# Kernel optimization log

Measured on AMD Instinct MI355X. Metric: run time of the kernel, lower is better.

The kernel has to match this reference:

```python
import jax, jax.numpy as jnp
import numpy as np

N_EMBD = 126
N_HEADS = 6
HEAD_DIM = N_EMBD // N_HEADS  # 21


def setup_inputs() -> dict:
    key = jax.random.key(0)
    k1, k2, k3 = jax.random.split(key, 3)
    B, T = 8, 2048
    x = jax.random.normal(k1, (B, T, N_EMBD), dtype=jnp.float32)
    # torch Linear weights stored as (out, in); we store transposed (in, out) for x @ W
    w_attn = jax.random.normal(k2, (N_EMBD, 3 * N_EMBD), dtype=jnp.float32) * (1.0 / np.sqrt(N_EMBD))
    w_proj = jax.random.normal(k3, (N_EMBD, N_EMBD), dtype=jnp.float32) * (1.0 / np.sqrt(N_EMBD))
    return {"x": x, "w_attn": w_attn, "w_proj": w_proj}


def reference(x, w_attn, w_proj):
    B, T, C = x.shape
    qkv = x @ w_attn                      # [B, T, 3C]
    q, k, v = jnp.split(qkv, 3, axis=-1)  # each [B, T, C]

    def heads(t):  # [B,T,C] -> [B,H,T,hd]
        return t.reshape(B, T, N_HEADS, HEAD_DIM).transpose(0, 2, 1, 3)

    q, k, v = heads(q), heads(k), heads(v)
    scale = 1.0 / np.sqrt(HEAD_DIM).astype(np.float32)
    scores = jnp.einsum('bhqd,bhkd->bhqk', q, k) * scale  # [B,H,T,T]
    causal = jnp.tril(jnp.ones((T, T), dtype=bool))
    scores = jnp.where(causal, scores, jnp.finfo(scores.dtype).min)
    attn = jax.nn.softmax(scores, axis=-1)
    out = jnp.einsum('bhqk,bhkd->bhqd', attn, v)           # [B,H,T,hd]
    out = out.transpose(0, 2, 1, 3).reshape(B, T, C)
    return out @ w_proj
```

## Files before the change

kernel.cpp:

```cpp
#include <hip/hip_runtime.h>
#include <hip/hip_bf16.h>


#define B_ 8
#define T_ 2048
#define C_ 126
#define H_ 6
#define D_ 21
#define TC_ 378
#define KP_ 128
#define DP_ 32
#define M_ 16384
#define QSCALE 0.31481923469333463f

typedef __hip_bfloat16 bf16;
typedef __bf16 bf16_t;
typedef __bf16 bf16x8 __attribute__((ext_vector_type(8)));
typedef float f32x4 __attribute__((ext_vector_type(4)));

__device__ __forceinline__ float ldf(const bf16* p, long i) { return __bfloat162float(p[i]); }
__device__ __forceinline__ float ldf(const float* p, long i) { return p[i]; }
__device__ __forceinline__ void stf(bf16* p, long i, float v) { p[i] = __float2bfloat16(v); }
__device__ __forceinline__ void stf(float* p, long i, float v) { p[i] = v; }

__device__ __forceinline__ unsigned int ld2(const bf16* x, long i) {
  return *(const unsigned int*)((const unsigned short*)x + i);
}
__device__ __forceinline__ unsigned int ld2(const float* x, long i) {
  const float2 f = *(const float2*)(x + i);
  union { bf16_t b[2]; unsigned int u; } cv;
  cv.b[0] = (bf16_t)f.x; cv.b[1] = (bf16_t)f.y;
  return cv.u;
}

__device__ __forceinline__ void probe_dtype(const void* x, int tid, int* sflag) {
  if (tid < 64) {
    const unsigned int w = ((const unsigned int*)x)[tid * 97 + 13];
    const unsigned int e = (w >> 7) & 0xFF;
    const bool bflike = (e >= 115 && e <= 131) || ((w & 0x7FFFu) == 0);
    const unsigned long long mask = __ballot(bflike);
    if (tid == 0) *sflag = (__popcll(mask) >= 40) ? 1 : 0;
  }
  __syncthreads();
}

template <typename T>
__device__ __forceinline__ void prep_w_body(const T* __restrict__ wa,
                                            const T* __restrict__ wp,
                                            bf16_t* __restrict__ WTa,
                                            bf16_t* __restrict__ WTp) {
  const int stride = gridDim.x * blockDim.x;
  const int idx0 = blockIdx.x * blockDim.x + threadIdx.x;
  for (int i = idx0; i < 384 * KP_ + KP_ * KP_; i += stride) {
    if (i < 384 * KP_) {
      const int n = i >> 7, k = i & 127;
      WTa[i] = (k < C_ && n < TC_) ? (bf16_t)ldf(wa, (long)k * TC_ + n) : (bf16_t)0.f;
    } else {
      const int j = i - 384 * KP_;
      const int n = j >> 7, k = j & 127;
      WTp[j] = (k < C_ && n < C_) ? (bf16_t)ldf(wp, (long)k * C_ + n) : (bf16_t)0.f;
    }
  }
}

__global__ __launch_bounds__(256) void prep_w_kernel(
    const void* __restrict__ x, const void* __restrict__ wa,
    const void* __restrict__ wp, bf16_t* __restrict__ WTa,
    bf16_t* __restrict__ WTp) {
  __shared__ int sflag;
  probe_dtype(x, threadIdx.x, &sflag);
  if (sflag) prep_w_body<bf16>((const bf16*)wa, (const bf16*)wp, WTa, WTp);
  else       prep_w_body<float>((const float*)wa, (const float*)wp, WTa, WTp);
}

#define QS_ 40

template <typename T>
__device__ __forceinline__ void qkv_body(
    const T* __restrict__ x, const bf16_t* __restrict__ WT,
    bf16_t* __restrict__ Qb, bf16_t* __restrict__ Kb, bf16_t* __restrict__ VT,
    bf16_t* __restrict__ xs, bf16_t* __restrict__ qbuf,
    bf16_t* __restrict__ kbuf, bf16_t* __restrict__ vbuf) {
  const int m0 = blockIdx.x * 16;
  const int tid = threadIdx.x;
  for (int i = tid; i < 16 * 64; i += 256) {
    const int row = i >> 6, cp = i & 63;
    unsigned int v = 0;
    if (cp < 63) v = ld2(x, (long)(m0 + row) * C_ + 2 * cp);
    ((unsigned int*)xs)[i] = v;
  }
  for (int i = tid; i < 6 * 16 * 11; i += 256) {
    const int h = i / 176, rem = i - h * 176, t = rem / 11, d = 21 + rem % 11;
    qbuf[(h * 16 + t) * QS_ + d] = (bf16_t)0.f;
    kbuf[(h * 16 + t) * QS_ + d] = (bf16_t)0.f;
  }
  for (int i = tid; i < 6 * 11 * 16; i += 256) {
    const int h = i / 176, rem = i - h * 176, d = 21 + rem / 16, t = rem % 16;
    vbuf[(h * 32 + d) * 16 + t] = (d == 21) ? (bf16_t)1.f : (bf16_t)0.f;
  }
  __syncthreads();

  const int wv = tid >> 6, lane = tid & 63;
  const int lr = lane & 15, quad = lane >> 4;
  const bf16_t* ar = xs + lr * KP_ + quad * 8;
  const bf16x8 a0 = *(const bf16x8*)(ar);
  const bf16x8 a1 = *(const bf16x8*)(ar + 32);
  const bf16x8 a2 = *(const bf16x8*)(ar + 64);
  const bf16x8 a3 = *(const bf16x8*)(ar + 96);

  for (int nt = wv; nt < 24; nt += 4) {
    const int n0 = nt * 16;
    const bf16x8* bp = (const bf16x8*)(WT + (long)(n0 + lr) * KP_ + quad * 8);
    f32x4 acc = {0.f, 0.f, 0.f, 0.f};
    acc = __builtin_amdgcn_mfma_f32_16x16x32_bf16(a0, bp[0],  acc, 0, 0, 0);
    acc = __builtin_amdgcn_mfma_f32_16x16x32_bf16(a1, bp[4],  acc, 0, 0, 0);
    acc = __builtin_amdgcn_mfma_f32_16x16x32_bf16(a2, bp[8],  acc, 0, 0, 0);
    acc = __builtin_amdgcn_mfma_f32_16x16x32_bf16(a3, bp[12], acc, 0, 0, 0);

    const int c = n0 + lr;
    if (c < TC_) {
      const int which = c / C_;
      const int cc = c - which * C_;
      const int h = cc / D_, d = cc - h * D_;
#pragma unroll
      for (int r = 0; r < 4; ++r) {
        const int t = quad * 4 + r;
        if (which == 0)
          qbuf[(h * 16 + t) * QS_ + d] = (bf16_t)(acc[r] * QSCALE);
        else if (which == 1)
          kbuf[(h * 16 + t) * QS_ + d] = (bf16_t)acc[r];
        else
          vbuf[(h * 32 + d) * 16 + t] = (bf16_t)acc[r];
      }
    }
  }
  __syncthreads();

  const int b = m0 >> 11, t0 = m0 & 2047;
  for (int i = tid; i < 192; i += 256) {
    const int j = (i < 96) ? i : i - 96;
    const int h = j >> 4, t = j & 15;
    const int4* src = (const int4*)(((i < 96) ? qbuf : kbuf) + (h * 16 + t) * QS_);
    int4* dst = (int4*)((((i < 96) ? Qb : Kb)) + ((long)(b * H_ + h) * T_ + (t0 + t)) * DP_);
    dst[0] = src[0]; dst[1] = src[1]; dst[2] = src[2]; dst[3] = src[3];
  }
  for (int i = tid; i < 192; i += 256) {
    const int h = i >> 5, d = i & 31;
    const int4* src = (const int4*)(vbuf + (h * 32 + d) * 16);
    int4* dst = (int4*)(VT + ((long)(b * H_ + h) * DP_ + d) * T_ + t0);
    dst[0] = src[0]; dst[1] = src[1];
  }
}

__global__ __launch_bounds__(256) void qkv_mfma(
    const void* __restrict__ x, const bf16_t* __restrict__ WT,
    bf16_t* __restrict__ Qb, bf16_t* __restrict__ Kb, bf16_t* __restrict__ VT) {
  __shared__ __align__(16) bf16_t xs[16 * KP_];
  __shared__ __align__(16) bf16_t qbuf[6 * 16 * QS_];
  __shared__ __align__(16) bf16_t kbuf[6 * 16 * QS_];
  __shared__ __align__(16) bf16_t vbuf[6 * 32 * 16];
  __shared__ int sflag;
  probe_dtype(x, threadIdx.x, &sflag);
  if (sflag) qkv_body<bf16>((const bf16*)x, WT, Qb, Kb, VT, xs, qbuf, kbuf, vbuf);
  else       qkv_body<float>((const float*)x, WT, Qb, Kb, VT, xs, qbuf, kbuf, vbuf);
}

__global__ __launch_bounds__(256, 4) void attn_mfma(
    const bf16_t* __restrict__ Qb, const bf16_t* __restrict__ Kb,
    const bf16_t* __restrict__ VT, bf16_t* __restrict__ ATTp) {
  __shared__ __align__(16) float smem[4352];
  const int bh = blockIdx.x;
  const int pr = 63 - blockIdx.y;
  const int tid = threadIdx.x;
  const int wv = tid >> 6, lane = tid & 63;
  const int lr = lane & 15, quad = lane >> 4;
  const int q0 = pr * 32;
  const int mq = quad * 4;

  const bf16_t* Qbh = Qb + (long)bh * T_ * DP_;
  const bf16_t* Kbh = Kb + (long)bh * T_ * DP_;
  const bf16_t* VTbh = VT + (long)bh * DP_ * T_;

  const bf16x8 qf0 = *(const bf16x8*)(Qbh + (long)(q0 + lr) * DP_ + quad * 8);
  const bf16x8 qf1 = *(const bf16x8*)(Qbh + (long)(q0 + 16 + lr) * DP_ + quad * 8);

  f32x4 o00 = {0.f,0.f,0.f,0.f}, o01 = {0.f,0.f,0.f,0.f};
  f32x4 o10 = {0.f,0.f,0.f,0.f}, o11 = {0.f,0.f,0.f,0.f};
  bf16_t* plA0 = (bf16_t*)smem + wv * 2048;
  bf16_t* plA1 = plA0 + 512;
  bf16_t* plB0 = plA0 + 1024;
  bf16_t* plB1 = plA0 + 1536;
  const int rsw = ((lane ^ (lane >> 2)) << 3);
  const int wb0 = ((lr >> 3) << 4) + mq;

  int t = wv;
  for (; t + 4 <= pr; t += 8) {
    const int kbA = t * 32, kbB = (t + 4) * 32;
    const bf16x8 kA0 = *(const bf16x8*)(Kbh + (long)(kbA + lr) * DP_ + quad * 8);
    const bf16x8 kA1 = *(const bf16x8*)(Kbh + (long)(kbA + 16 + lr) * DP_ + quad * 8);
    const bf16x8 kB0 = *(const bf16x8*)(Kbh + (long)(kbB + lr) * DP_ + quad * 8);
    const bf16x8 kB1 = *(const bf16x8*)(Kbh + (long)(kbB + 16 + lr) * DP_ + quad * 8);
    const bf16x8 vA0 = *(const bf16x8*)(VTbh + (long)lr * T_ + kbA + quad * 8);
    const bf16x8 vA1 = *(const bf16x8*)(VTbh + (long)(16 + lr) * T_ + kbA + quad * 8);
    const bf16x8 vB0 = *(const bf16x8*)(VTbh + (long)lr * T_ + kbB + quad * 8);
    const bf16x8 vB1 = *(const bf16x8*)(VTbh + (long)(16 + lr) * T_ + kbB + quad * 8);

    f32x4 sA00 = {0.f,0.f,0.f,0.f}, sA01 = {0.f,0.f,0.f,0.f};
    f32x4 sA10 = {0.f,0.f,0.f,0.f}, sA11 = {0.f,0.f,0.f,0.f};
    f32x4 sB00 = {0.f,0.f,0.f,0.f}, sB01 = {0.f,0.f,0.f,0.f};
    f32x4 sB10 = {0.f,0.f,0.f,0.f}, sB11 = {0.f,0.f,0.f,0.f};
    sA00 = __builtin_amdgcn_mfma_f32_16x16x32_bf16(qf0, kA0, sA00, 0, 0, 0);
    sA01 = __builtin_amdgcn_mfma_f32_16x16x32_bf16(qf0, kA1, sA01, 0, 0, 0);
    sA10 = __builtin_amdgcn_mfma_f32_16x16x32_bf16(qf1, kA0, sA10, 0, 0, 0);
    sA11 = __builtin_amdgcn_mfma_f32_16x16x32_bf16(qf1, kA1, sA11, 0, 0, 0);
    sB00 = __builtin_amdgcn_mfma_f32_16x16x32_bf16(qf0, kB0, sB00, 0, 0, 0);
    sB01 = __builtin_amdgcn_mfma_f32_16x16x32_bf16(qf0, kB1, sB01, 0, 0, 0);
    sB10 = __builtin_amdgcn_mfma_f32_16x16x32_bf16(qf1, kB0, sB10, 0, 0, 0);
    sB11 = __builtin_amdgcn_mfma_f32_16x16x32_bf16(qf1, kB1, sB11, 0, 0, 0);

    if (t + 4 == pr) {
#pragma unroll
      for (int r = 0; r < 4; ++r) {
        if (lr > mq + r) { sB00[r] = -1e30f; sB11[r] = -1e30f; }
        sB01[r] = -1e30f;
      }
    }
#pragma unroll
    for (int r = 0; r < 4; ++r) {
      const int b0 = wb0 + r, b1 = b0 + 32;
      const int i0 = ((b0 ^ (b0 >> 2)) << 3) + (lr & 7);
      const int i1 = ((b1 ^ (b1 >> 2)) << 3) + (lr & 7);
      plA0[i0] = (bf16_t)exp2f(sA00[r]);
      plA0[i1] = (bf16_t)exp2f(sA01[r]);
      plA1[i0] = (bf16_t)exp2f(sA10[r]);
      plA1[i1] = (bf16_t)exp2f(sA11[r]);
      plB0[i0] = (bf16_t)exp2f(sB00[r]);
      plB0[i1] = (bf16_t)exp2f(sB01[r]);
      plB1[i0] = (bf16_t)exp2f(sB10[r]);
      plB1[i1] = (bf16_t)exp2f(sB11[r]);
    }
    __builtin_amdgcn_wave_barrier();
    const bf16x8 pfA0 = *(const bf16x8*)(plA0 + rsw);
    const bf16x8 pfA1 = *(const bf16x8*)(plA1 + rsw);
    const bf16x8 pfB0 = *(const bf16x8*)(plB0 + rsw);
    const bf16x8 pfB1 = *(const bf16x8*)(plB1 + rsw);
    __builtin_amdgcn_wave_barrier();

    o00 = __builtin_amdgcn_mfma_f32_16x16x32_bf16(pfA0, vA0, o00, 0, 0, 0);
    o01 = __builtin_amdgcn_mfma_f32_16x16x32_bf16(pfA0, vA1, o01, 0, 0, 0);
    o10 = __builtin_amdgcn_mfma_f32_16x16x32_bf16(pfA1, vA0, o10, 0, 0, 0);
    o11 = __builtin_amdgcn_mfma_f32_16x16x32_bf16(pfA1, vA1, o11, 0, 0, 0);
    o00 = __builtin_amdgcn_mfma_f32_16x16x32_bf16(pfB0, vB0, o00, 0, 0, 0);
    o01 = __builtin_amdgcn_mfma_f32_16x16x32_bf16(pfB0, vB1, o01, 0, 0, 0);
    o10 = __builtin_amdgcn_mfma_f32_16x16x32_bf16(pfB1, vB0, o10, 0, 0, 0);
    o11 = __builtin_amdgcn_mfma_f32_16x16x32_bf16(pfB1, vB1, o11, 0, 0, 0);
  }

  if (t <= pr) {
    const int kb = t * 32;
    const bf16x8 k0 = *(const bf16x8*)(Kbh + (long)(kb + lr) * DP_ + quad * 8);
    const bf16x8 k1 = *(const bf16x8*)(Kbh + (long)(kb + 16 + lr) * DP_ + quad * 8);
    const bf16x8 v0 = *(const bf16x8*)(VTbh + (long)lr * T_ + kb + quad * 8);
    const bf16x8 v1 = *(const bf16x8*)(VTbh + (long)(16 + lr) * T_ + kb + quad * 8);
    f32x4 s00 = {0.f,0.f,0.f,0.f}, s01 = {0.f,0.f,0.f,0.f};
    f32x4 s10 = {0.f,0.f,0.f,0.f}, s11 = {0.f,0.f,0.f,0.f};
    s00 = __builtin_amdgcn_mfma_f32_16x16x32_bf16(qf0, k0, s00, 0, 0, 0);
    s01 = __builtin_amdgcn_mfma_f32_16x16x32_bf16(qf0, k1, s01, 0, 0, 0);
    s10 = __builtin_amdgcn_mfma_f32_16x16x32_bf16(qf1, k0, s10, 0, 0, 0);
    s11 = __builtin_amdgcn_mfma_f32_16x16x32_bf16(qf1, k1, s11, 0, 0, 0);
    if (t == pr) {
#pragma unroll
      for (int r = 0; r < 4; ++r) {
        if (lr > mq + r) { s00[r] = -1e30f; s11[r] = -1e30f; }
        s01[r] = -1e30f;
      }
    }
#pragma unroll
    for (int r = 0; r < 4; ++r) {
      const int b0 = wb0 + r, b1 = b0 + 32;
      const int i0 = ((b0 ^ (b0 >> 2)) << 3) + (lr & 7);
      const int i1 = ((b1 ^ (b1 >> 2)) << 3) + (lr & 7);
      plA0[i0] = (bf16_t)exp2f(s00[r]);
      plA0[i1] = (bf16_t)exp2f(s01[r]);
      plA1[i0] = (bf16_t)exp2f(s10[r]);
      plA1[i1] = (bf16_t)exp2f(s11[r]);
    }
    __builtin_amdgcn_wave_barrier();
    const bf16x8 pf0 = *(const bf16x8*)(plA0 + rsw);
    const bf16x8 pf1 = *(const bf16x8*)(plA1 + rsw);
    __builtin_amdgcn_wave_barrier();
    o00 = __builtin_amdgcn_mfma_f32_16x16x32_bf16(pf0, v0, o00, 0, 0, 0);
    o01 = __builtin_amdgcn_mfma_f32_16x16x32_bf16(pf0, v1, o01, 0, 0, 0);
    o10 = __builtin_amdgcn_mfma_f32_16x16x32_bf16(pf1, v0, o10, 0, 0, 0);
    o11 = __builtin_amdgcn_mfma_f32_16x16x32_bf16(pf1, v1, o11, 0, 0, 0);
  }

  __syncthreads();
  {
    float* my = smem + (wv * 64 + lane) * 17;
#pragma unroll
    for (int j = 0; j < 4; ++j) {
      my[j]      = o00[j];
      my[4 + j]  = o01[j];
      my[8 + j]  = o10[j];
      my[12 + j] = o11[j];
    }
  }
  __syncthreads();

  if (wv == 0) {
    float tot[16];
#pragma unroll
    for (int j = 0; j < 16; ++j)
      tot[j] = smem[lane * 17 + j] + smem[(64 + lane) * 17 + j] +
               smem[(128 + lane) * 17 + j] + smem[(192 + lane) * 17 + j];
    const int b = bh / H_, h = bh - b * H_;
#pragma unroll
    for (int r = 0; r < 4; ++r) {
      const float rl0 = 1.f / __shfl(tot[4 + r],  (lane & 48) + 5, 64);
      const float rl1 = 1.f / __shfl(tot[12 + r], (lane & 48) + 5, 64);
      const int qA = q0 + mq + r, qB = qA + 16;
      bf16_t* opA = ATTp + (long)(b * T_ + qA) * KP_ + h * D_;
      bf16_t* opB = ATTp + (long)(b * T_ + qB) * KP_ + h * D_;
      opA[lr] = (bf16_t)(tot[r] * rl0);
      opB[lr] = (bf16_t)(tot[8 + r] * rl1);
      if (lr < 5) {
        opA[16 + lr] = (bf16_t)(tot[4 + r] * rl0);
        opB[16 + lr] = (bf16_t)(tot[12 + r] * rl1);
      }
    }
  }
}

__global__ __launch_bounds__(256) void proj_mfma(
    const void* __restrict__ x, const bf16_t* __restrict__ ATTp,
    const bf16_t* __restrict__ WT, void* __restrict__ out) {
  __shared__ int sflag;
  probe_dtype(x, threadIdx.x, &sflag);
  const int isbf = sflag;

  const int m0 = blockIdx.x * 16;
  const int tid = threadIdx.x;
  const int wv = tid >> 6, lane = tid & 63;
  const int lr = lane & 15, quad = lane >> 4;

  const bf16x8* ap = (const bf16x8*)(ATTp + (long)(m0 + lr) * KP_ + quad * 8);
  const bf16x8 a0 = ap[0], a1 = ap[4], a2 = ap[8], a3 = ap[12];

  for (int nt = wv; nt < 8; nt += 4) {
    const int n0 = nt * 16;
    const bf16x8* bp = (const bf16x8*)(WT + (long)(n0 + lr) * KP_ + quad * 8);
    f32x4 acc = {0.f, 0.f, 0.f, 0.f};
    acc = __builtin_amdgcn_mfma_f32_16x16x32_bf16(a0, bp[0],  acc, 0, 0, 0);
    acc = __builtin_amdgcn_mfma_f32_16x16x32_bf16(a1, bp[4],  acc, 0, 0, 0);
    acc = __builtin_amdgcn_mfma_f32_16x16x32_bf16(a2, bp[8],  acc, 0, 0, 0);
    acc = __builtin_amdgcn_mfma_f32_16x16x32_bf16(a3, bp[12], acc, 0, 0, 0);

    const int c = n0 + lr;
    if (c < C_) {
#pragma unroll
      for (int r = 0; r < 4; ++r) {
        const int m = m0 + quad * 4 + r;
        if (isbf) stf((bf16*)out,  (long)m * C_ + c, acc[r]);
        else      stf((float*)out, (long)m * C_ + c, acc[r]);
      }
    }
  }
}

extern "C" void kernel_launch(void* const* d_in, const int* in_sizes, int n_in,
                              void* d_out, int out_size, void* d_ws, size_t ws_size,
                              hipStream_t stream) {
  const void* x      = d_in[0];
  const void* w_attn = d_in[1];
  const void* w_proj = d_in[2];

  char* base = (char*)d_ws;
  const long QKV = (long)48 * T_ * DP_;
  bf16_t* Qb = (bf16_t*)(base + 256);
  bf16_t* Kb = Qb + QKV;
  bf16_t* VT = Kb + QKV;
  bf16_t* WTa  = VT + QKV;
  bf16_t* WTp  = WTa + 384 * KP_;
  bf16_t* ATTp = WTp + KP_ * KP_;

  prep_w_kernel<<<64, 256, 0, stream>>>(x, w_attn, w_proj, WTa, WTp);
  qkv_mfma<<<M_ / 16, 256, 0, stream>>>(x, WTa, Qb, Kb, VT);
  attn_mfma<<<dim3(48, 64), 256, 0, stream>>>(Qb, Kb, VT, ATTp);
  proj_mfma<<<M_ / 16, 256, 0, stream>>>(x, ATTp, WTp, d_out);
}
```

Measured before the change: 135.4 us.

## Enlarge qkv/proj row tiles, stage proj output in LDS, tile weight transpose

The weight-prep kernel now transposes via a padded shared-memory tile so global reads and writes are coalesced. The QKV kernel processes 32 rows per block instead of 16, halving the block count and reusing weight fetches across two M tiles. The projection kernel handles 64 rows per block, stages results in LDS and writes contiguous vectorized output. The staging rounds fp32 outputs to bf16, which loses precision for float outputs.

```diff
diff --git a/kernel.cpp b/kernel.cpp
--- a/kernel.cpp
+++ b/kernel.cpp
@@ -48,18 +48,31 @@
 __device__ __forceinline__ void prep_w_body(const T* __restrict__ wa,
                                             const T* __restrict__ wp,
                                             bf16_t* __restrict__ WTa,
-                                            bf16_t* __restrict__ WTp) {
-  const int stride = gridDim.x * blockDim.x;
-  const int idx0 = blockIdx.x * blockDim.x + threadIdx.x;
-  for (int i = idx0; i < 384 * KP_ + KP_ * KP_; i += stride) {
-    if (i < 384 * KP_) {
-      const int n = i >> 7, k = i & 127;
-      WTa[i] = (k < C_ && n < TC_) ? (bf16_t)ldf(wa, (long)k * TC_ + n) : (bf16_t)0.f;
-    } else {
-      const int j = i - 384 * KP_;
-      const int n = j >> 7, k = j & 127;
-      WTp[j] = (k < C_ && n < C_) ? (bf16_t)ldf(wp, (long)k * C_ + n) : (bf16_t)0.f;
-    }
+                                            bf16_t* __restrict__ WTp,
+                                            float (*tile)[65]) {
+  const int id = blockIdx.x;
+  const bool isA = id < 12;
+  const int nt = isA ? (id % 6) : ((id - 12) & 1);
+  const int kt = isA ? (id / 6) : ((id - 12) >> 1);
+  const T* src = isA ? wa : wp;
+  bf16_t* dst = isA ? WTa : WTp;
+  const int NN = isA ? TC_ : C_;
+  const int NR = isA ? 384 : KP_;
+  const int tid = threadIdx.x;
+  const int wv = tid >> 6, lane = tid & 63;
+
+#pragma unroll
+  for (int rr = 0; rr < 16; ++rr) {
+    const int kl = wv * 16 + rr;
+    const int k = kt * 64 + kl, n = nt * 64 + lane;
+    tile[kl][lane] = (k < C_ && n < NN) ? ldf(src, (long)k * NN + n) : 0.f;
+  }
+  __syncthreads();
+#pragma unroll
+  for (int rr = 0; rr < 16; ++rr) {
+    const int nl = wv * 16 + rr;
+    const int n = nt * 64 + nl;
+    if (n < NR) dst[(long)n * KP_ + kt * 64 + lane] = (bf16_t)tile[lane][nl];
   }
 }
 
@@ -67,10 +80,11 @@
     const void* __restrict__ x, const void* __restrict__ wa,
     const void* __restrict__ wp, bf16_t* __restrict__ WTa,
     bf16_t* __restrict__ WTp) {
+  __shared__ float tile[64][65];
   __shared__ int sflag;
   probe_dtype(x, threadIdx.x, &sflag);
-  if (sflag) prep_w_body<bf16>((const bf16*)wa, (const bf16*)wp, WTa, WTp);
-  else       prep_w_body<float>((const float*)wa, (const float*)wp, WTa, WTp);
+  if (sflag) prep_w_body<bf16>((const bf16*)wa, (const bf16*)wp, WTa, WTp, tile);
+  else       prep_w_body<float>((const float*)wa, (const float*)wp, WTa, WTp, tile);
 }
 
 #define QS_ 40
@@ -81,34 +95,35 @@
     bf16_t* __restrict__ Qb, bf16_t* __restrict__ Kb, bf16_t* __restrict__ VT,
     bf16_t* __restrict__ xs, bf16_t* __restrict__ qbuf,
     bf16_t* __restrict__ kbuf, bf16_t* __restrict__ vbuf) {
-  const int m0 = blockIdx.x * 16;
+  const int m0 = blockIdx.x * 32;
   const int tid = threadIdx.x;
-  for (int i = tid; i < 16 * 64; i += 256) {
+  for (int i = tid; i < 32 * 64; i += 256) {
     const int row = i >> 6, cp = i & 63;
     unsigned int v = 0;
     if (cp < 63) v = ld2(x, (long)(m0 + row) * C_ + 2 * cp);
     ((unsigned int*)xs)[i] = v;
   }
-  for (int i = tid; i < 6 * 16 * 11; i += 256) {
-    const int h = i / 176, rem = i - h * 176, t = rem / 11, d = 21 + rem % 11;
-    qbuf[(h * 16 + t) * QS_ + d] = (bf16_t)0.f;
-    kbuf[(h * 16 + t) * QS_ + d] = (bf16_t)0.f;
-  }
-  for (int i = tid; i < 6 * 11 * 16; i += 256) {
-    const int h = i / 176, rem = i - h * 176, d = 21 + rem / 16, t = rem % 16;
-    vbuf[(h * 32 + d) * 16 + t] = (d == 21) ? (bf16_t)1.f : (bf16_t)0.f;
+  for (int i = tid; i < 6 * 32 * 11; i += 256) {
+    const int h = i / 352, rem = i - h * 352, t = rem / 11, d = 21 + rem % 11;
+    qbuf[(h * 32 + t) * QS_ + d] = (bf16_t)0.f;
+    kbuf[(h * 32 + t) * QS_ + d] = (bf16_t)0.f;
+  }
+  for (int i = tid; i < 6 * 11 * 32; i += 256) {
+    const int h = i / 352, rem = i - h * 352, d = 21 + rem / 32, t = rem & 31;
+    vbuf[(h * 32 + d) * 32 + t] = (d == 21) ? (bf16_t)1.f : (bf16_t)0.f;
   }
   __syncthreads();
 
   const int wv = tid >> 6, lane = tid & 63;
   const int lr = lane & 15, quad = lane >> 4;
-  const bf16_t* ar = xs + lr * KP_ + quad * 8;
+  const int mt = wv >> 1;
+  const bf16_t* ar = xs + (mt * 16 + lr) * KP_ + quad * 8;
   const bf16x8 a0 = *(const bf16x8*)(ar);
   const bf16x8 a1 = *(const bf16x8*)(ar + 32);
   const bf16x8 a2 = *(const bf16x8*)(ar + 64);
   const bf16x8 a3 = *(const bf16x8*)(ar + 96);
 
-  for (int nt = wv; nt < 24; nt += 4) {
+  for (int nt = (wv & 1); nt < 24; nt += 2) {
     const int n0 = nt * 16;
     const bf16x8* bp = (const bf16x8*)(WT + (long)(n0 + lr) * KP_ + quad * 8);
     f32x4 acc = {0.f, 0.f, 0.f, 0.f};
@@ -124,41 +139,41 @@
       const int h = cc / D_, d = cc - h * D_;
 #pragma unroll
       for (int r = 0; r < 4; ++r) {
-        const int t = quad * 4 + r;
+        const int t = mt * 16 + quad * 4 + r;
         if (which == 0)
-          qbuf[(h * 16 + t) * QS_ + d] = (bf16_t)(acc[r] * QSCALE);
+          qbuf[(h * 32 + t) * QS_ + d] = (bf16_t)(acc[r] * QSCALE);
         else if (which == 1)
-          kbuf[(h * 16 + t) * QS_ + d] = (bf16_t)acc[r];
+          kbuf[(h * 32 + t) * QS_ + d] = (bf16_t)acc[r];
         else
-          vbuf[(h * 32 + d) * 16 + t] = (bf16_t)acc[r];
+          vbuf[(h * 32 + d) * 32 + t] = (bf16_t)acc[r];
       }
     }
   }
   __syncthreads();
 
   const int b = m0 >> 11, t0 = m0 & 2047;
-  for (int i = tid; i < 192; i += 256) {
-    const int j = (i < 96) ? i : i - 96;
-    const int h = j >> 4, t = j & 15;
-    const int4* src = (const int4*)(((i < 96) ? qbuf : kbuf) + (h * 16 + t) * QS_);
-    int4* dst = (int4*)((((i < 96) ? Qb : Kb)) + ((long)(b * H_ + h) * T_ + (t0 + t)) * DP_);
+  for (int i = tid; i < 384; i += 256) {
+    const int j = (i < 192) ? i : i - 192;
+    const int h = j >> 5, t = j & 31;
+    const int4* src = (const int4*)(((i < 192) ? qbuf : kbuf) + (h * 32 + t) * QS_);
+    int4* dst = (int4*)((((i < 192) ? Qb : Kb)) + ((long)(b * H_ + h) * T_ + (t0 + t)) * DP_);
     dst[0] = src[0]; dst[1] = src[1]; dst[2] = src[2]; dst[3] = src[3];
   }
   for (int i = tid; i < 192; i += 256) {
     const int h = i >> 5, d = i & 31;
-    const int4* src = (const int4*)(vbuf + (h * 32 + d) * 16);
+    const int4* src = (const int4*)(vbuf + (h * 32 + d) * 32);
     int4* dst = (int4*)(VT + ((long)(b * H_ + h) * DP_ + d) * T_ + t0);
-    dst[0] = src[0]; dst[1] = src[1];
+    dst[0] = src[0]; dst[1] = src[1]; dst[2] = src[2]; dst[3] = src[3];
   }
 }
 
 __global__ __launch_bounds__(256) void qkv_mfma(
     const void* __restrict__ x, const bf16_t* __restrict__ WT,
     bf16_t* __restrict__ Qb, bf16_t* __restrict__ Kb, bf16_t* __restrict__ VT) {
-  __shared__ __align__(16) bf16_t xs[16 * KP_];
-  __shared__ __align__(16) bf16_t qbuf[6 * 16 * QS_];
-  __shared__ __align__(16) bf16_t kbuf[6 * 16 * QS_];
-  __shared__ __align__(16) bf16_t vbuf[6 * 32 * 16];
+  __shared__ __align__(16) bf16_t xs[32 * KP_];
+  __shared__ __align__(16) bf16_t qbuf[6 * 32 * QS_];
+  __shared__ __align__(16) bf16_t kbuf[6 * 32 * QS_];
+  __shared__ __align__(16) bf16_t vbuf[6 * 32 * 32];
   __shared__ int sflag;
   probe_dtype(x, threadIdx.x, &sflag);
   if (sflag) qkv_body<bf16>((const bf16*)x, WT, Qb, Kb, VT, xs, qbuf, kbuf, vbuf);
@@ -332,22 +347,25 @@
   }
 }
 
+#define OS_ 136
 __global__ __launch_bounds__(256) void proj_mfma(
     const void* __restrict__ x, const bf16_t* __restrict__ ATTp,
     const bf16_t* __restrict__ WT, void* __restrict__ out) {
+  __shared__ __align__(16) bf16_t obuf[64 * OS_];
   __shared__ int sflag;
   probe_dtype(x, threadIdx.x, &sflag);
   const int isbf = sflag;
 
-  const int m0 = blockIdx.x * 16;
+  const int m0 = blockIdx.x * 64;
   const int tid = threadIdx.x;
   const int wv = tid >> 6, lane = tid & 63;
   const int lr = lane & 15, quad = lane >> 4;
 
-  const bf16x8* ap = (const bf16x8*)(ATTp + (long)(m0 + lr) * KP_ + quad * 8);
+  const bf16x8* ap = (const bf16x8*)(ATTp + (long)(m0 + wv * 16 + lr) * KP_ + quad * 8);
   const bf16x8 a0 = ap[0], a1 = ap[4], a2 = ap[8], a3 = ap[12];
 
-  for (int nt = wv; nt < 8; nt += 4) {
+#pragma unroll
+  for (int nt = 0; nt < 8; ++nt) {
     const int n0 = nt * 16;
     const bf16x8* bp = (const bf16x8*)(WT + (long)(n0 + lr) * KP_ + quad * 8);
     f32x4 acc = {0.f, 0.f, 0.f, 0.f};
@@ -355,15 +373,23 @@
     acc = __builtin_amdgcn_mfma_f32_16x16x32_bf16(a1, bp[4],  acc, 0, 0, 0);
     acc = __builtin_amdgcn_mfma_f32_16x16x32_bf16(a2, bp[8],  acc, 0, 0, 0);
     acc = __builtin_amdgcn_mfma_f32_16x16x32_bf16(a3, bp[12], acc, 0, 0, 0);
-
-    const int c = n0 + lr;
-    if (c < C_) {
-#pragma unroll
-      for (int r = 0; r < 4; ++r) {
-        const int m = m0 + quad * 4 + r;
-        if (isbf) stf((bf16*)out,  (long)m * C_ + c, acc[r]);
-        else      stf((float*)out, (long)m * C_ + c, acc[r]);
-      }
+#pragma unroll
+    for (int r = 0; r < 4; ++r)
+      obuf[(wv * 16 + quad * 4 + r) * OS_ + n0 + lr] = (bf16_t)acc[r];
+  }
+  __syncthreads();
+
+  for (int i = tid; i < 64 * 63; i += 256) {
+    const int row = i / 63, c2 = i - row * 63;
+    const bf16_t* s = obuf + row * OS_ + 2 * c2;
+    if (isbf) {
+      union { bf16_t b[2]; unsigned int u; } cv;
+      cv.b[0] = s[0]; cv.b[1] = s[1];
+      ((unsigned int*)out)[(long)(m0 + row) * 63 + c2] = cv.u;
+    } else {
+      float2 f;
+      f.x = (float)s[0]; f.y = (float)s[1];
+      ((float2*)out)[(long)(m0 + row) * 63 + c2] = f;
     }
   }
 }
@@ -384,8 +410,8 @@
   bf16_t* WTp  = WTa + 384 * KP_;
   bf16_t* ATTp = WTp + KP_ * KP_;
 
-  prep_w_kernel<<<64, 256, 0, stream>>>(x, w_attn, w_proj, WTa, WTp);
-  qkv_mfma<<<M_ / 16, 256, 0, stream>>>(x, WTa, Qb, Kb, VT);
+  prep_w_kernel<<<16, 256, 0, stream>>>(x, w_attn, w_proj, WTa, WTp);
+  qkv_mfma<<<M_ / 32, 256, 0, stream>>>(x, WTa, Qb, Kb, VT);
   attn_mfma<<<dim3(48, 64), 256, 0, stream>>>(Qb, Kb, VT, ATTp);
-  proj_mfma<<<M_ / 16, 256, 0, stream>>>(x, ATTp, WTp, d_out);
-}
+  proj_mfma<<<M_ / 64, 256, 0, stream>>>(x, ATTp, WTp, d_out);
+}
```

After: 141.8 us. 1.05x slower.

## Pair causal query tiles per block for balanced work and cheaper bf16 rounding

Applied to the files above, without the earlier changes.

Each attention block now handles two query tiles, pr = 63-y and pr = y, so every block does roughly the same amount of causal work, and the grid is halved to 48x32. This targets the load imbalance and tail effect that came from giving short and long causal rows to separate blocks. The P-matrix conversion also switches from the bf16 cast to a hand-written round-half-up bit trick (no NaN handling) written as ushort into shared memory. The cost is fewer blocks in flight, a serial pass over both tiles, and an extra barrier between the passes.

```diff
diff --git a/kernel.cpp b/kernel.cpp
--- a/kernel.cpp
+++ b/kernel.cpp
@@ -12,6 +12,7 @@
 #define DP_ 32
 #define M_ 16384
 #define QSCALE 0.31481923469333463f
+#define QS_ 40
 
 typedef __hip_bfloat16 bf16;
 typedef __bf16 bf16_t;
@@ -31,6 +32,11 @@
   union { bf16_t b[2]; unsigned int u; } cv;
   cv.b[0] = (bf16_t)f.x; cv.b[1] = (bf16_t)f.y;
   return cv.u;
+}
+
+__device__ __forceinline__ unsigned short f2b(float f) {
+  union { float f; unsigned int u; } v; v.f = f;
+  return (unsigned short)((v.u + 0x8000u) >> 16);
 }
 
 __device__ __forceinline__ void probe_dtype(const void* x, int tid, int* sflag) {
@@ -73,8 +79,6 @@
   else       prep_w_body<float>((const float*)wa, (const float*)wp, WTa, WTp);
 }
 
-#define QS_ 40
-
 template <typename T>
 __device__ __forceinline__ void qkv_body(
     const T* __restrict__ x, const bf16_t* __restrict__ WT,
@@ -170,165 +174,173 @@
     const bf16_t* __restrict__ VT, bf16_t* __restrict__ ATTp) {
   __shared__ __align__(16) float smem[4352];
   const int bh = blockIdx.x;
-  const int pr = 63 - blockIdx.y;
+  const int cc_ = blockIdx.y;
   const int tid = threadIdx.x;
   const int wv = tid >> 6, lane = tid & 63;
   const int lr = lane & 15, quad = lane >> 4;
-  const int q0 = pr * 32;
   const int mq = quad * 4;
 
   const bf16_t* Qbh = Qb + (long)bh * T_ * DP_;
   const bf16_t* Kbh = Kb + (long)bh * T_ * DP_;
   const bf16_t* VTbh = VT + (long)bh * DP_ * T_;
 
-  const bf16x8 qf0 = *(const bf16x8*)(Qbh + (long)(q0 + lr) * DP_ + quad * 8);
-  const bf16x8 qf1 = *(const bf16x8*)(Qbh + (long)(q0 + 16 + lr) * DP_ + quad * 8);
-
-  f32x4 o00 = {0.f,0.f,0.f,0.f}, o01 = {0.f,0.f,0.f,0.f};
-  f32x4 o10 = {0.f,0.f,0.f,0.f}, o11 = {0.f,0.f,0.f,0.f};
-  bf16_t* plA0 = (bf16_t*)smem + wv * 2048;
-  bf16_t* plA1 = plA0 + 512;
-  bf16_t* plB0 = plA0 + 1024;
-  bf16_t* plB1 = plA0 + 1536;
+  unsigned short* plA0 = (unsigned short*)smem + wv * 2048;
+  unsigned short* plA1 = plA0 + 512;
+  unsigned short* plB0 = plA0 + 1024;
+  unsigned short* plB1 = plA0 + 1536;
   const int rsw = ((lane ^ (lane >> 2)) << 3);
   const int wb0 = ((lr >> 3) << 4) + mq;
 
-  int t = wv;
-  for (; t + 4 <= pr; t += 8) {
-    const int kbA = t * 32, kbB = (t + 4) * 32;
-    const bf16x8 kA0 = *(const bf16x8*)(Kbh + (long)(kbA + lr) * DP_ + quad * 8);
-    const bf16x8 kA1 = *(const bf16x8*)(Kbh + (long)(kbA + 16 + lr) * DP_ + quad * 8);
-    const bf16x8 kB0 = *(const bf16x8*)(Kbh + (long)(kbB + lr) * DP_ + quad * 8);
-    const bf16x8 kB1 = *(const bf16x8*)(Kbh + (long)(kbB + 16 + lr) * DP_ + quad * 8);
-    const bf16x8 vA0 = *(const bf16x8*)(VTbh + (long)lr * T_ + kbA + quad * 8);
-    const bf16x8 vA1 = *(const bf16x8*)(VTbh + (long)(16 + lr) * T_ + kbA + quad * 8);
-    const bf16x8 vB0 = *(const bf16x8*)(VTbh + (long)lr * T_ + kbB + quad * 8);
-    const bf16x8 vB1 = *(const bf16x8*)(VTbh + (long)(16 + lr) * T_ + kbB + quad * 8);
-
-    f32x4 sA00 = {0.f,0.f,0.f,0.f}, sA01 = {0.f,0.f,0.f,0.f};
-    f32x4 sA10 = {0.f,0.f,0.f,0.f}, sA11 = {0.f,0.f,0.f,0.f};
-    f32x4 sB00 = {0.f,0.f,0.f,0.f}, sB01 = {0.f,0.f,0.f,0.f};
-    f32x4 sB10 = {0.f,0.f,0.f,0.f}, sB11 = {0.f,0.f,0.f,0.f};
-    sA00 = __builtin_amdgcn_mfma_f32_16x16x32_bf16(qf0, kA0, sA00, 0, 0, 0);
-    sA01 = __builtin_amdgcn_mfma_f32_16x16x32_bf16(qf0, kA1, sA01, 0, 0, 0);
-    sA10 = __builtin_amdgcn_mfma_f32_16x16x32_bf16(qf1, kA0, sA10, 0, 0, 0);
-    sA11 = __builtin_amdgcn_mfma_f32_16x16x32_bf16(qf1, kA1, sA11, 0, 0, 0);
-    sB00 = __builtin_amdgcn_mfma_f32_16x16x32_bf16(qf0, kB0, sB00, 0, 0, 0);
-    sB01 = __builtin_amdgcn_mfma_f32_16x16x32_bf16(qf0, kB1, sB01, 0, 0, 0);
-    sB10 = __builtin_amdgcn_mfma_f32_16x16x32_bf16(qf1, kB0, sB10, 0, 0, 0);
-    sB11 = __builtin_amdgcn_mfma_f32_16x16x32_bf16(qf1, kB1, sB11, 0, 0, 0);
-
-    if (t + 4 == pr) {
+  const int prs[2] = {63 - cc_, cc_};
+#pragma unroll
+  for (int uj = 0; uj < 2; ++uj) {
+    const int pr = prs[uj];
+    const int q0 = pr * 32;
+
+    const bf16x8 qf0 = *(const bf16x8*)(Qbh + (long)(q0 + lr) * DP_ + quad * 8);
+    const bf16x8 qf1 = *(const bf16x8*)(Qbh + (long)(q0 + 16 + lr) * DP_ + quad * 8);
+
+    f32x4 o00 = {0.f,0.f,0.f,0.f}, o01 = {0.f,0.f,0.f,0.f};
+    f32x4 o10 = {0.f,0.f,0.f,0.f}, o11 = {0.f,0.f,0.f,0.f};
+
+    int t = wv;
+    for (; t + 4 <= pr; t += 8) {
+      const int kbA = t * 32, kbB = (t + 4) * 32;
+      const bf16x8 kA0 = *(const bf16x8*)(Kbh + (long)(kbA + lr) * DP_ + quad * 8);
+      const bf16x8 kA1 = *(const bf16x8*)(Kbh + (long)(kbA + 16 + lr) * DP_ + quad * 8);
+      const bf16x8 kB0 = *(const bf16x8*)(Kbh + (long)(kbB + lr) * DP_ + quad * 8);
+      const bf16x8 kB1 = *(const bf16x8*)(Kbh + (long)(kbB + 16 + lr) * DP_ + quad * 8);
+      const bf16x8 vA0 = *(const bf16x8*)(VTbh + (long)lr * T_ + kbA + quad * 8);
+      const bf16x8 vA1 = *(const bf16x8*)(VTbh + (long)(16 + lr) * T_ + kbA + quad * 8);
+      const bf16x8 vB0 = *(const bf16x8*)(VTbh + (long)lr * T_ + kbB + quad * 8);
+      const bf16x8 vB1 = *(const bf16x8*)(VTbh + (long)(16 + lr) * T_ + kbB + quad * 8);
+
+      f32x4 sA00 = {0.f,0.f,0.f,0.f}, sA01 = {0.f,0.f,0.f,0.f};
+      f32x4 sA10 = {0.f,0.f,0.f,0.f}, sA11 = {0.f,0.f,0.f,0.f};
+      f32x4 sB00 = {0.f,0.f,0.f,0.f}, sB01 = {0.f,0.f,0.f,0.f};
+      f32x4 sB10 = {0.f,0.f,0.f,0.f}, sB11 = {0.f,0.f,0.f,0.f};
+      sA00 = __builtin_amdgcn_mfma_f32_16x16x32_bf16(qf0, kA0, sA00, 0, 0, 0);
+      sA01 = __builtin_amdgcn_mfma_f32_16x16x32_bf16(qf0, kA1, sA01, 0, 0, 0);
+      sA10 = __builtin_amdgcn_mfma_f32_16x16x32_bf16(qf1, kA0, sA10, 0, 0, 0);
+      sA11 = __builtin_amdgcn_mfma_f32_16x16x32_bf16(qf1, kA1, sA11, 0, 0, 0);
+      sB00 = __builtin_amdgcn_mfma_f32_16x16x32_bf16(qf0, kB0, sB00, 0, 0, 0);
+      sB01 = __builtin_amdgcn_mfma_f32_16x16x32_bf16(qf0, kB1, sB01, 0, 0, 0);
+      sB10 = __builtin_amdgcn_mfma_f32_16x16x32_bf16(qf1, kB0, sB10, 0, 0, 0);
+      sB11 = __builtin_amdgcn_mfma_f32_16x16x32_bf16(qf1, kB1, sB11, 0, 0, 0);
+
+      if (t + 4 == pr) {
+#pragma unroll
+        for (int r = 0; r < 4; ++r) {
+          if (lr > mq + r) { sB00[r] = -1e30f; sB11[r] = -1e30f; }
+          sB01[r] = -1e30f;
+        }
+      }
 #pragma unroll
       for (int r = 0; r < 4; ++r) {
-        if (lr > mq + r) { sB00[r] = -1e30f; sB11[r] = -1e30f; }
-        sB01[r] = -1e30f;
-      }
-    }
-#pragma unroll
-    for (int r = 0; r < 4; ++r) {
-      const int b0 = wb0 + r, b1 = b0 + 32;
-      const int i0 = ((b0 ^ (b0 >> 2)) << 3) + (lr & 7);
-      const int i1 = ((b1 ^ (b1 >> 2)) << 3) + (lr & 7);
-      plA0[i0] = (bf16_t)exp2f(sA00[r]);
-      plA0[i1] = (bf16_t)exp2f(sA01[r]);
-      plA1[i0] = (bf16_t)exp2f(sA10[r]);
-      plA1[i1] = (bf16_t)exp2f(sA11[r]);
-      plB0[i0] = (bf16_t)exp2f(sB00[r]);
-      plB0[i1] = (bf16_t)exp2f(sB01[r]);
-      plB1[i0] = (bf16_t)exp2f(sB10[r]);
-      plB1[i1] = (bf16_t)exp2f(sB11[r]);
-    }
-    __builtin_amdgcn_wave_barrier();
-    const bf16x8 pfA0 = *(const bf16x8*)(plA0 + rsw);
-    const bf16x8 pfA1 = *(const bf16x8*)(plA1 + rsw);
-    const bf16x8 pfB0 = *(const bf16x8*)(plB0 + rsw);
-    const bf16x8 pfB1 = *(const bf16x8*)(plB1 + rsw);
-    __builtin_amdgcn_wave_barrier();
-
-    o00 = __builtin_amdgcn_mfma_f32_16x16x32_bf16(pfA0, vA0, o00, 0, 0, 0);
-    o01 = __builtin_amdgcn_mfma_f32_16x16x32_bf16(pfA0, vA1, o01, 0, 0, 0);
-    o10 = __builtin_amdgcn_mfma_f32_16x16x32_bf16(pfA1, vA0, o10, 0, 0, 0);
-    o11 = __builtin_amdgcn_mfma_f32_16x16x32_bf16(pfA1, vA1, o11, 0, 0, 0);
-    o00 = __builtin_amdgcn_mfma_f32_16x16x32_bf16(pfB0, vB0, o00, 0, 0, 0);
-    o01 = __builtin_amdgcn_mfma_f32_16x16x32_bf16(pfB0, vB1, o01, 0, 0, 0);
-    o10 = __builtin_amdgcn_mfma_f32_16x16x32_bf16(pfB1, vB0, o10, 0, 0, 0);
-    o11 = __builtin_amdgcn_mfma_f32_16x16x32_bf16(pfB1, vB1, o11, 0, 0, 0);
-  }
-
-  if (t <= pr) {
-    const int kb = t * 32;
-    const bf16x8 k0 = *(const bf16x8*)(Kbh + (long)(kb + lr) * DP_ + quad * 8);
-    const bf16x8 k1 = *(const bf16x8*)(Kbh + (long)(kb + 16 + lr) * DP_ + quad * 8);
-    const bf16x8 v0 = *(const bf16x8*)(VTbh + (long)lr * T_ + kb + quad * 8);
-    const bf16x8 v1 = *(const bf16x8*)(VTbh + (long)(16 + lr) * T_ + kb + quad * 8);
-    f32x4 s00 = {0.f,0.f,0.f,0.f}, s01 = {0.f,0.f,0.f,0.f};
-    f32x4 s10 = {0.f,0.f,0.f,0.f}, s11 = {0.f,0.f,0.f,0.f};
-    s00 = __builtin_amdgcn_mfma_f32_16x16x32_bf16(qf0, k0, s00, 0, 0, 0);
-    s01 = __builtin_amdgcn_mfma_f32_16x16x32_bf16(qf0, k1, s01, 0, 0, 0);
-    s10 = __builtin_amdgcn_mfma_f32_16x16x32_bf16(qf1, k0, s10, 0, 0, 0);
-    s11 = __builtin_amdgcn_mfma_f32_16x16x32_bf16(qf1, k1, s11, 0, 0, 0);
-    if (t == pr) {
+        const int b0 = wb0 + r, b1 = b0 + 32;
+        const int i0 = ((b0 ^ (b0 >> 2)) << 3) + (lr & 7);
+        const int i1 = ((b1 ^ (b1 >> 2)) << 3) + (lr & 7);
+        plA0[i0] = f2b(exp2f(sA00[r]));
+        plA0[i1] = f2b(exp2f(sA01[r]));
+        plA1[i0] = f2b(exp2f(sA10[r]));
+        plA1[i1] = f2b(exp2f(sA11[r]));
+        plB0[i0] = f2b(exp2f(sB00[r]));
+        plB0[i1] = f2b(exp2f(sB01[r]));
+        plB1[i0] = f2b(exp2f(sB10[r]));
+        plB1[i1] = f2b(exp2f(sB11[r]));
+      }
+      __builtin_amdgcn_wave_barrier();
+      const bf16x8 pfA0 = *(const bf16x8*)(plA0 + rsw);
+      const bf16x8 pfA1 = *(const bf16x8*)(plA1 + rsw);
+      const bf16x8 pfB0 = *(const bf16x8*)(plB0 + rsw);
+      const bf16x8 pfB1 = *(const bf16x8*)(plB1 + rsw);
+      __builtin_amdgcn_wave_barrier();
+
+      o00 = __builtin_amdgcn_mfma_f32_16x16x32_bf16(pfA0, vA0, o00, 0, 0, 0);
+      o01 = __builtin_amdgcn_mfma_f32_16x16x32_bf16(pfA0, vA1, o01, 0, 0, 0);
+      o10 = __builtin_amdgcn_mfma_f32_16x16x32_bf16(pfA1, vA0, o10, 0, 0, 0);
+      o11 = __builtin_amdgcn_mfma_f32_16x16x32_bf16(pfA1, vA1, o11, 0, 0, 0);
+      o00 = __builtin_amdgcn_mfma_f32_16x16x32_bf16(pfB0, vB0, o00, 0, 0, 0);
+      o01 = __builtin_amdgcn_mfma_f32_16x16x32_bf16(pfB0, vB1, o01, 0, 0, 0);
+      o10 = __builtin_amdgcn_mfma_f32_16x16x32_bf16(pfB1, vB0, o10, 0, 0, 0);
+      o11 = __builtin_amdgcn_mfma_f32_16x16x32_bf16(pfB1, vB1, o11, 0, 0, 0);
+    }
+
+    if (t <= pr) {
+      const int kb = t * 32;
+      const bf16x8 k0 = *(const bf16x8*)(Kbh + (long)(kb + lr) * DP_ + quad * 8);
+      const bf16x8 k1 = *(const bf16x8*)(Kbh + (long)(kb + 16 + lr) * DP_ + quad * 8);
+      const bf16x8 v0 = *(const bf16x8*)(VTbh + (long)lr * T_ + kb + quad * 8);
+      const bf16x8 v1 = *(const bf16x8*)(VTbh + (long)(16 + lr) * T_ + kb + quad * 8);
+      f32x4 s00 = {0.f,0.f,0.f,0.f}, s01 = {0.f,0.f,0.f,0.f};
+      f32x4 s10 = {0.f,0.f,0.f,0.f}, s11 = {0.f,0.f,0.f,0.f};
+      s00 = __builtin_amdgcn_mfma_f32_16x16x32_bf16(qf0, k0, s00, 0, 0, 0);
+      s01 = __builtin_amdgcn_mfma_f32_16x16x32_bf16(qf0, k1, s01, 0, 0, 0);
+      s10 = __builtin_amdgcn_mfma_f32_16x16x32_bf16(qf1, k0, s10, 0, 0, 0);
+      s11 = __builtin_amdgcn_mfma_f32_16x16x32_bf16(qf1, k1, s11, 0, 0, 0);
+      if (t == pr) {
+#pragma unroll
+        for (int r = 0; r < 4; ++r) {
+          if (lr > mq + r) { s00[r] = -1e30f; s11[r] = -1e30f; }
+          s01[r] = -1e30f;
+        }
+      }
 #pragma unroll
       for (int r = 0; r < 4; ++r) {
-        if (lr > mq + r) { s00[r] = -1e30f; s11[r] = -1e30f; }
-        s01[r] = -1e30f;
-      }
-    }
-#pragma unroll
-    for (int r = 0; r < 4; ++r) {
-      const int b0 = wb0 + r, b1 = b0 + 32;
-      const int i0 = ((b0 ^ (b0 >> 2)) << 3) + (lr & 7);
-      const int i1 = ((b1 ^ (b1 >> 2)) << 3) + (lr & 7);
-      plA0[i0] = (bf16_t)exp2f(s00[r]);
-      plA0[i1] = (bf16_t)exp2f(s01[r]);
-      plA1[i0] = (bf16_t)exp2f(s10[r]);
-      plA1[i1] = (bf16_t)exp2f(s11[r]);
-    }
-    __builtin_amdgcn_wave_barrier();
-    const bf16x8 pf0 = *(const bf16x8*)(plA0 + rsw);
-    const bf16x8 pf1 = *(const bf16x8*)(plA1 + rsw);
-    __builtin_amdgcn_wave_barrier();
-    o00 = __builtin_amdgcn_mfma_f32_16x16x32_bf16(pf0, v0, o00, 0, 0, 0);
-    o01 = __builtin_amdgcn_mfma_f32_16x16x32_bf16(pf0, v1, o01, 0, 0, 0);
-    o10 = __builtin_amdgcn_mfma_f32_16x16x32_bf16(pf1, v0, o10, 0, 0, 0);
-    o11 = __builtin_amdgcn_mfma_f32_16x16x32_bf16(pf1, v1, o11, 0, 0, 0);
-  }
-
-  __syncthreads();
-  {
-    float* my = smem + (wv * 64 + lane) * 17;
-#pragma unroll
-    for (int j = 0; j < 4; ++j) {
-      my[j]      = o00[j];
-      my[4 + j]  = o01[j];
-      my[8 + j]  = o10[j];
-      my[12 + j] = o11[j];
-    }
-  }
-  __syncthreads();
-
-  if (wv == 0) {
-    float tot[16];
-#pragma unroll
-    for (int j = 0; j < 16; ++j)
-      tot[j] = smem[lane * 17 + j] + smem[(64 + lane) * 17 + j] +
-               smem[(128 + lane) * 17 + j] + smem[(192 + lane) * 17 + j];
-    const int b = bh / H_, h = bh - b * H_;
-#pragma unroll
-    for (int r = 0; r < 4; ++r) {
-      const float rl0 = 1.f / __shfl(tot[4 + r],  (lane & 48) + 5, 64);
-      const float rl1 = 1.f / __shfl(tot[12 + r], (lane & 48) + 5, 64);
-      const int qA = q0 + mq + r, qB = qA + 16;
-      bf16_t* opA = ATTp + (long)(b * T_ + qA) * KP_ + h * D_;
-      bf16_t* opB = ATTp + (long)(b * T_ + qB) * KP_ + h * D_;
-      opA[lr] = (bf16_t)(tot[r] * rl0);
-      opB[lr] = (bf16_t)(tot[8 + r] * rl1);
-      if (lr < 5) {
-        opA[16 + lr] = (bf16_t)(tot[4 + r] * rl0);
-        opB[16 + lr] = (bf16_t)(tot[12 + r] * rl1);
-      }
-    }
+        const int b0 = wb0 + r, b1 = b0 + 32;
+        const int i0 = ((b0 ^ (b0 >> 2)) << 3) + (lr & 7);
+        const int i1 = ((b1 ^ (b1 >> 2)) << 3) + (lr & 7);
+        plA0[i0] = f2b(exp2f(s00[r]));
+        plA0[i1] = f2b(exp2f(s01[r]));
+        plA1[i0] = f2b(exp2f(s10[r]));
+        plA1[i1] = f2b(exp2f(s11[r]));
+      }
+      __builtin_amdgcn_wave_barrier();
+      const bf16x8 pf0 = *(const bf16x8*)(plA0 + rsw);
+      const bf16x8 pf1 = *(const bf16x8*)(plA1 + rsw);
+      __builtin_amdgcn_wave_barrier();
+      o00 = __builtin_amdgcn_mfma_f32_16x16x32_bf16(pf0, v0, o00, 0, 0, 0);
+      o01 = __builtin_amdgcn_mfma_f32_16x16x32_bf16(pf0, v1, o01, 0, 0, 0);
+      o10 = __builtin_amdgcn_mfma_f32_16x16x32_bf16(pf1, v0, o10, 0, 0, 0);
+      o11 = __builtin_amdgcn_mfma_f32_16x16x32_bf16(pf1, v1, o11, 0, 0, 0);
+    }
+
+    __syncthreads();
+    {
+      float* my = smem + (wv * 64 + lane) * 17;
+#pragma unroll
+      for (int j = 0; j < 4; ++j) {
+        my[j]      = o00[j];
+        my[4 + j]  = o01[j];
+        my[8 + j]  = o10[j];
+        my[12 + j] = o11[j];
+      }
+    }
+    __syncthreads();
+
+    if (wv == 0) {
+      float tot[16];
+#pragma unroll
+      for (int j = 0; j < 16; ++j)
+        tot[j] = smem[lane * 17 + j] + smem[(64 + lane) * 17 + j] +
+                 smem[(128 + lane) * 17 + j] + smem[(192 + lane) * 17 + j];
+      const int b = bh / H_, h = bh - b * H_;
+#pragma unroll
+      for (int r = 0; r < 4; ++r) {
+        const float rl0 = 1.f / __shfl(tot[4 + r],  (lane & 48) + 5, 64);
+        const float rl1 = 1.f / __shfl(tot[12 + r], (lane & 48) + 5, 64);
+        const int qA = q0 + mq + r, qB = qA + 16;
+        bf16_t* opA = ATTp + (long)(b * T_ + qA) * KP_ + h * D_;
+        bf16_t* opB = ATTp + (long)(b * T_ + qB) * KP_ + h * D_;
+        opA[lr] = (bf16_t)(tot[r] * rl0);
+        opB[lr] = (bf16_t)(tot[8 + r] * rl1);
+        if (lr < 5) {
+          opA[16 + lr] = (bf16_t)(tot[4 + r] * rl0);
+          opB[16 + lr] = (bf16_t)(tot[12 + r] * rl1);
+        }
+      }
+    }
+    __syncthreads();
   }
 }
 
@@ -386,6 +398,6 @@
 
   prep_w_kernel<<<64, 256, 0, stream>>>(x, w_attn, w_proj, WTa, WTp);
   qkv_mfma<<<M_ / 16, 256, 0, stream>>>(x, WTa, Qb, Kb, VT);
-  attn_mfma<<<dim3(48, 64), 256, 0, stream>>>(Qb, Kb, VT, ATTp);
+  attn_mfma<<<dim3(48, 32), 256, 0, stream>>>(Qb, Kb, VT, ATTp);
   proj_mfma<<<M_ / 16, 256, 0, stream>>>(x, ATTp, WTp, d_out);
 }
```

Result: slower. 140.3 us (+3.6%).
